# Optimization experiments

Measured on AMD Instinct MI355X. Metric: run time of the kernel, lower is better.

## Reference

```python
import jax, jax.numpy as jnp
import numpy as np

BATCH, SEQ, D_IN, D_OUT = 32, 1024, 128, 128
NEG_SLOPE = 0.1


def setup_inputs() -> dict:
    key = jax.random.key(0)
    k1, k2, k3, k4 = jax.random.split(key, 4)
    nodes = jax.random.normal(k1, (BATCH, SEQ, D_IN), dtype=jnp.float32)
    adjacent = jax.random.randint(k2, (BATCH, SEQ, SEQ), 0, 2, dtype=jnp.int32)
    W = jax.random.normal(k3, (D_IN, D_OUT), dtype=jnp.float32) / np.sqrt(D_IN)
    B = jax.random.normal(k4, (D_IN, D_OUT), dtype=jnp.float32) / np.sqrt(D_IN)
    return {"nodes": nodes, "adjacent": adjacent, "W": W, "B": B}


def reference(nodes, adjacent, W, B):
    # mask[b, out, in] = 1 if edge (out -> in) present
    mask = (adjacent != 0).astype(nodes.dtype)
    # counts[b, in] = in-degree (number of 'out' neighbors pooled per target node)
    counts = mask.sum(axis=1)                               # [b, s_in]
    # segment-sum of neighbor features: pooled[b, in, d] = sum_out mask * nodes[b, out, d]
    pooled = jnp.einsum('boi,bod->bid', mask, nodes)        # [b, s_in, d]
    # mean over neighbors; nodes with zero degree get no pooled contribution
    pooled = jnp.where(counts[..., None] > 0,
                       pooled / jnp.maximum(counts, 1.0)[..., None],
                       jnp.zeros((), dtype=nodes.dtype))
    updated = nodes @ B + pooled @ W                        # [b, s, d_out]
    return jax.nn.leaky_relu(updated, negative_slope=NEG_SLOPE)
```

## Files before the change

### kernel.cpp

```cpp
#include <hip/hip_runtime.h>
#include <hip/hip_bf16.h>

#define SEQ 1024
#define DIM 128
#define NEG_SLOPE 0.1f

typedef __bf16 bf16x8 __attribute__((ext_vector_type(8)));
typedef float f32x4v __attribute__((ext_vector_type(4)));
typedef unsigned char uchar;

#define NTQ_BYTES ((size_t)32 * 128 * 1024)

__device__ __forceinline__ unsigned short bfb(float f) {
    __bf16 h = (__bf16)f;
    return __builtin_bit_cast(unsigned short, h);
}

__device__ __forceinline__ uchar f32_to_e4m3(float f) {
#if __has_builtin(__builtin_amdgcn_cvt_pk_fp8_f32)
    int r = __builtin_amdgcn_cvt_pk_fp8_f32(f, f, 0, false);
    return (uchar)(r & 0xff);
#else
    unsigned u = __builtin_bit_cast(unsigned, f);
    unsigned s = (u >> 24) & 0x80;
    int e = (u >> 23) & 0xff;
    unsigned m = u & 0x7fffff;
    int te = e - 120;
    if (te >= 1) {
        unsigned keep = m >> 20, rest = m & 0xfffff;
        keep += (rest > 0x80000u) || (rest == 0x80000u && (keep & 1));
        if (keep == 8) { keep = 0; ++te; }
        if (te > 15) return (uchar)(s | 0x7e);
        return (uchar)(s | (te << 3) | keep);
    }
    float af = f < 0 ? -f : f;
    int q = (int)(af * 512.0f + 0.5f);
    if (q > 7) q = 7;
    return (uchar)(s | q);
#endif
}

__device__ __forceinline__ long mk64(unsigned lo, unsigned hi) {
    return (long)(((unsigned long long)hi << 32) | lo);
}

__global__ __launch_bounds__(256)
void transpose_nodes(const float* __restrict__ nodes, uchar* __restrict__ nq)
{
    __shared__ float lds[64][33];
    const int b  = blockIdx.x >> 6;
    const int ot = (blockIdx.x >> 2) & 15;
    const int dt = blockIdx.x & 3;
    const int o0 = ot << 6, d0 = dt << 5;
    const int t  = threadIdx.x;

    const float* src = nodes + ((size_t)(b * SEQ + o0)) * DIM + d0;
    #pragma unroll
    for (int p = 0; p < 8; ++p) {
        const int o = (t >> 5) + p * 8;
        const int d = t & 31;
        lds[o][d] = src[(size_t)o * DIM + d];
    }
    __syncthreads();

    const int d_loc = t >> 3;
    const int p0    = (t & 7) * 8;
    union { uchar b[8]; uint2 u; } pk;
    #pragma unroll
    for (int j = 0; j < 8; ++j) pk.b[j] = f32_to_e4m3(lds[p0 + j][d_loc]);
    *(uint2*)(nq + ((size_t)(b * DIM + d0 + d_loc)) * SEQ + o0 + p0) = pk.u;
}

__global__ __launch_bounds__(256)
void transpose_wb(const float* __restrict__ W, const float* __restrict__ Bm,
                  unsigned short* __restrict__ wt, unsigned short* __restrict__ bt)
{
    const int which = blockIdx.x & 1;
    const int slice = blockIdx.x >> 1;
    const float* in = which ? Bm : W;
    unsigned short* out = which ? bt : wt;
    const int base = slice * 1024;
    #pragma unroll
    for (int r = 0; r < 4; ++r) {
        const int idx = base + r * 256 + threadIdx.x;
        const int d = idx >> 7, k = idx & 127;
        out[idx] = bfb(in[k * DIM + d]);
    }
}

__global__ __launch_bounds__(256, 4)
void gcn_main(const float* __restrict__ nodes,
              const int* __restrict__ adj,
              const uchar* __restrict__ nq,
              const unsigned short* __restrict__ wt,
              const unsigned short* __restrict__ bt,
              float* __restrict__ out)
{
    __shared__ __align__(16) uchar mask_t[2][32][80];
    __shared__ unsigned short pooled[32][136];

    const int bid   = blockIdx.x;
    const int xcd   = bid & 7;
    const int slot  = bid >> 3;
    const int batch = ((slot >> 5) << 3) | xcd;
    const int itile = slot & 31;
    const int i0    = itile << 5;

    const int tid  = threadIdx.x;
    const int wave = tid >> 6;
    const int lane = tid & 63;
    const int wh   = wave >> 1;
    const int wn   = wave & 1;
    const int lrow = lane & 15;
    const int quad = lane >> 4;

    const int*   __restrict__ adj_b   = adj   + (size_t)batch * SEQ * SEQ;
    const uchar* __restrict__ nq_b    = nq    + (size_t)batch * DIM * SEQ;
    const float* __restrict__ nodes_b = nodes + (size_t)batch * SEQ * DIM;

    const int ig = tid & 15;
    const int og = tid >> 4;

    f32x4v acc[4] = {};
    f32x4v acc_cnt = {};
    const long ones = 0x3838383838383838L;

    int2 A[4];
    auto load_adj = [&](int oc) {
        const int* pa = adj_b + (size_t)(oc + og * 4) * SEQ + i0 + ig * 2;
        #pragma unroll
        for (int rr = 0; rr < 4; ++rr) A[rr] = *(const int2*)(pa + (size_t)rr * SEQ);
    };
    uint4 Bv[4];
    const uchar* pb0 = nq_b + (size_t)(wn * 64 + lrow) * SEQ + quad * 16;
    auto load_B = [&](int off) {
        #pragma unroll
        for (int nf = 0; nf < 4; ++nf)
            Bv[nf] = *(const uint4*)(pb0 + (size_t)nf * 16 * SEQ + off);
    };

    load_adj(0);
    load_B(0);

    for (int n = 0; n < 16; ++n) {
        const int buf = n & 1;
        unsigned w0 = 0, w1 = 0;
        #pragma unroll
        for (int rr = 0; rr < 4; ++rr) {
            w0 |= (A[rr].x != 0 ? 0x38u : 0u) << (8 * rr);
            w1 |= (A[rr].y != 0 ? 0x38u : 0u) << (8 * rr);
        }
        *(unsigned*)&mask_t[buf][ig * 2][og * 4]     = w0;
        *(unsigned*)&mask_t[buf][ig * 2 + 1][og * 4] = w1;
        __syncthreads();

        uint4 Bc[4];
        #pragma unroll
        for (int nf = 0; nf < 4; ++nf) Bc[nf] = Bv[nf];
        if (n < 15) {
            load_adj((n + 1) * 64);
            load_B((n + 1) * 64);
        }

        const uint4 a4 = *(const uint4*)&mask_t[buf][wh * 16 + lrow][quad * 16];
        #pragma unroll
        for (int half = 0; half < 2; ++half) {
            const long a64 = half ? mk64(a4.z, a4.w) : mk64(a4.x, a4.y);
            #pragma unroll
            for (int nf = 0; nf < 4; ++nf) {
                const long b64 = half ? mk64(Bc[nf].z, Bc[nf].w) : mk64(Bc[nf].x, Bc[nf].y);
                acc[nf] = __builtin_amdgcn_mfma_f32_16x16x32_fp8_fp8(a64, b64, acc[nf], 0, 0, 0);
            }
            acc_cnt = __builtin_amdgcn_mfma_f32_16x16x32_fp8_fp8(a64, ones, acc_cnt, 0, 0, 0);
        }
    }

    #pragma unroll
    for (int r = 0; r < 4; ++r) {
        const int row = wh * 16 + quad * 4 + r;
        const float cnt = acc_cnt[r];
        const float inv = (cnt > 0.5f) ? 1.0f / cnt : 0.0f;
        #pragma unroll
        for (int nf = 0; nf < 4; ++nf) {
            const int col = wn * 64 + nf * 16 + lrow;
            pooled[row][col] = bfb(acc[nf][r] * inv);
        }
    }
    __syncthreads();

    f32x4v acc2[4] = {};
    const int d_b0 = wn * 64 + lrow;

    #pragma unroll
    for (int ks = 0; ks < 4; ++ks) {
        const int k0 = ks * 32 + quad * 8;
        bf16x8 av, av2, bw[4], bb[4];
        av = *(const bf16x8*)&pooled[wh * 16 + lrow][k0];
        {
            const float* p = nodes_b + (size_t)(i0 + wh * 16 + lrow) * DIM + k0;
            const float4 f1 = *(const float4*)p;
            const float4 f2 = *(const float4*)(p + 4);
            av2[0] = (__bf16)f1.x; av2[1] = (__bf16)f1.y;
            av2[2] = (__bf16)f1.z; av2[3] = (__bf16)f1.w;
            av2[4] = (__bf16)f2.x; av2[5] = (__bf16)f2.y;
            av2[6] = (__bf16)f2.z; av2[7] = (__bf16)f2.w;
        }
        #pragma unroll
        for (int nf = 0; nf < 4; ++nf) {
            bw[nf] = *(const bf16x8*)(wt + (size_t)(d_b0 + nf * 16) * DIM + k0);
            bb[nf] = *(const bf16x8*)(bt + (size_t)(d_b0 + nf * 16) * DIM + k0);
        }
        #pragma unroll
        for (int nf = 0; nf < 4; ++nf) {
            acc2[nf] = __builtin_amdgcn_mfma_f32_16x16x32_bf16(av,  bw[nf], acc2[nf], 0, 0, 0);
            acc2[nf] = __builtin_amdgcn_mfma_f32_16x16x32_bf16(av2, bb[nf], acc2[nf], 0, 0, 0);
        }
    }

    float* out_b = out + (size_t)batch * SEQ * DIM;
    #pragma unroll
    for (int nf = 0; nf < 4; ++nf) {
        const int col = wn * 64 + nf * 16 + lrow;
        #pragma unroll
        for (int r = 0; r < 4; ++r) {
            const int row = i0 + wh * 16 + quad * 4 + r;
            const float x = acc2[nf][r];
            out_b[(size_t)row * DIM + col] = (x > 0.0f) ? x : NEG_SLOPE * x;
        }
    }
}

extern "C" void kernel_launch(void* const* d_in, const int* in_sizes, int n_in,
                              void* d_out, int out_size, void* d_ws, size_t ws_size,
                              hipStream_t stream) {
    const float* nodes = (const float*)d_in[0];
    const int*   adj   = (const int*)d_in[1];
    const float* W     = (const float*)d_in[2];
    const float* Bm    = (const float*)d_in[3];
    float*       out   = (float*)d_out;

    uchar* nq = (uchar*)d_ws;
    unsigned short* wt = (unsigned short*)(nq + NTQ_BYTES);
    unsigned short* bt = wt + 16384;

    transpose_nodes<<<dim3(2048), dim3(256), 0, stream>>>(nodes, nq);
    transpose_wb   <<<dim3(32),   dim3(256), 0, stream>>>(W, Bm, wt, bt);
    gcn_main       <<<dim3(1024), dim3(256), 0, stream>>>(nodes, adj, nq, wt, bt, out);
}
```

Baseline: 248.3 us.

## Stage full adjacency mask tile in LDS upfront, removing per-iteration barriers

The kernel now reads the block's whole 1024x32 adjacency column slab in a first phase, using 16-byte int4 loads instead of int2. It converts the slab to fp8 mask bytes and stores it transposed in a single LDS buffer that is unioned with the pooled tile. The MFMA loop then runs fully unrolled with no __syncthreads and only double-buffers the nq operand from global memory. The aim is to cut the 16 barriers and the fine-grained interleaving of adjacency loads. In exchange, LDS use rises to about 33KB per block, which may lower occupancy, and the adjacency load phase no longer overlaps with the MFMA work.

Result: no change. 252.9 us (+1.9%).

```diff
diff --git a/kernel.cpp b/kernel.cpp
--- a/kernel.cpp
+++ b/kernel.cpp
@@ -96,8 +96,11 @@
               const unsigned short* __restrict__ bt,
               float* __restrict__ out)
 {
-    __shared__ __align__(16) uchar mask_t[2][32][80];
-    __shared__ unsigned short pooled[32][136];
+    union U {
+        uchar maskT[32][1040];
+        unsigned short pooled[32][136];
+    };
+    __shared__ __align__(16) U u;
 
     const int bid   = blockIdx.x;
     const int xcd   = bid & 7;
@@ -118,51 +121,57 @@
     const uchar* __restrict__ nq_b    = nq    + (size_t)batch * DIM * SEQ;
     const float* __restrict__ nodes_b = nodes + (size_t)batch * SEQ * DIM;
 
-    const int ig = tid & 15;
-    const int og = tid >> 4;
+    const int cg = tid & 7;
+    const int rg = tid >> 3;
+    const int* pa_base = adj_b + (size_t)(rg * 4) * SEQ + i0 + cg * 4;
+
+    int4 Acur[4], Anxt[4];
+    #pragma unroll
+    for (int r = 0; r < 4; ++r) Acur[r] = *(const int4*)(pa_base + (size_t)r * SEQ);
+
+    #pragma unroll
+    for (int p = 0; p < 8; ++p) {
+        if (p < 7) {
+            const int* pa = pa_base + (size_t)(p + 1) * 128 * SEQ;
+            #pragma unroll
+            for (int r = 0; r < 4; ++r) Anxt[r] = *(const int4*)(pa + (size_t)r * SEQ);
+        }
+        const int obase = p * 128 + rg * 4;
+        #pragma unroll
+        for (int c = 0; c < 4; ++c) {
+            unsigned w = 0;
+            w |= (((const int*)&Acur[0])[c] != 0 ? 0x38u : 0u);
+            w |= (((const int*)&Acur[1])[c] != 0 ? 0x38u : 0u) << 8;
+            w |= (((const int*)&Acur[2])[c] != 0 ? 0x38u : 0u) << 16;
+            w |= (((const int*)&Acur[3])[c] != 0 ? 0x38u : 0u) << 24;
+            *(unsigned*)&u.maskT[cg * 4 + c][obase] = w;
+        }
+        #pragma unroll
+        for (int r = 0; r < 4; ++r) Acur[r] = Anxt[r];
+    }
+    __syncthreads();
 
     f32x4v acc[4] = {};
     f32x4v acc_cnt = {};
     const long ones = 0x3838383838383838L;
 
-    int2 A[4];
-    auto load_adj = [&](int oc) {
-        const int* pa = adj_b + (size_t)(oc + og * 4) * SEQ + i0 + ig * 2;
-        #pragma unroll
-        for (int rr = 0; rr < 4; ++rr) A[rr] = *(const int2*)(pa + (size_t)rr * SEQ);
-    };
-    uint4 Bv[4];
     const uchar* pb0 = nq_b + (size_t)(wn * 64 + lrow) * SEQ + quad * 16;
-    auto load_B = [&](int off) {
-        #pragma unroll
-        for (int nf = 0; nf < 4; ++nf)
-            Bv[nf] = *(const uint4*)(pb0 + (size_t)nf * 16 * SEQ + off);
-    };
-
-    load_adj(0);
-    load_B(0);
-
+    const uchar* prow = &u.maskT[wh * 16 + lrow][quad * 16];
+
+    uint4 Bbuf[2][4];
+    #pragma unroll
+    for (int nf = 0; nf < 4; ++nf)
+        Bbuf[0][nf] = *(const uint4*)(pb0 + (size_t)nf * 16 * SEQ);
+
+    #pragma unroll
     for (int n = 0; n < 16; ++n) {
-        const int buf = n & 1;
-        unsigned w0 = 0, w1 = 0;
-        #pragma unroll
-        for (int rr = 0; rr < 4; ++rr) {
-            w0 |= (A[rr].x != 0 ? 0x38u : 0u) << (8 * rr);
-            w1 |= (A[rr].y != 0 ? 0x38u : 0u) << (8 * rr);
-        }
-        *(unsigned*)&mask_t[buf][ig * 2][og * 4]     = w0;
-        *(unsigned*)&mask_t[buf][ig * 2 + 1][og * 4] = w1;
-        __syncthreads();
-
-        uint4 Bc[4];
-        #pragma unroll
-        for (int nf = 0; nf < 4; ++nf) Bc[nf] = Bv[nf];
         if (n < 15) {
-            load_adj((n + 1) * 64);
-            load_B((n + 1) * 64);
-        }
-
-        const uint4 a4 = *(const uint4*)&mask_t[buf][wh * 16 + lrow][quad * 16];
+            #pragma unroll
+            for (int nf = 0; nf < 4; ++nf)
+                Bbuf[(n + 1) & 1][nf] = *(const uint4*)(pb0 + (size_t)nf * 16 * SEQ + (n + 1) * 64);
+        }
+        const uint4 a4 = *(const uint4*)(prow + n * 64);
+        const uint4* Bc = Bbuf[n & 1];
         #pragma unroll
         for (int half = 0; half < 2; ++half) {
             const long a64 = half ? mk64(a4.z, a4.w) : mk64(a4.x, a4.y);
@@ -175,6 +184,8 @@
         }
     }
 
+    __syncthreads();
+
     #pragma unroll
     for (int r = 0; r < 4; ++r) {
         const int row = wh * 16 + quad * 4 + r;
@@ -183,7 +194,7 @@
         #pragma unroll
         for (int nf = 0; nf < 4; ++nf) {
             const int col = wn * 64 + nf * 16 + lrow;
-            pooled[row][col] = bfb(acc[nf][r] * inv);
+            u.pooled[row][col] = bfb(acc[nf][r] * inv);
         }
     }
     __syncthreads();
@@ -195,7 +206,7 @@
     for (int ks = 0; ks < 4; ++ks) {
         const int k0 = ks * 32 + quad * 8;
         bf16x8 av, av2, bw[4], bb[4];
-        av = *(const bf16x8*)&pooled[wh * 16 + lrow][k0];
+        av = *(const bf16x8*)&u.pooled[wh * 16 + lrow][k0];
         {
             const float* p = nodes_b + (size_t)(i0 + wh * 16 + lrow) * DIM + k0;
             const float4 f1 = *(const float4*)p;
```

## Pre-quantize adjacency to transposed fp8 mask in a separate kernel

Applied to the files above, without the earlier changes.

Adds a quant_adj kernel that reads the int32 adjacency once and writes a transposed fp8 mask (0x38 for an edge, 0 otherwise) to workspace. gcn_main then loads the A fragments straight from this byte mask. That drops the in-loop LDS transpose, the per-iteration __syncthreads, and the 4-byte adjacency reads in the main loop, and the loop now uses a three-slot register prefetch for both operands. In exchange there is an extra launch, about 64MB of extra traffic (32MB fp8 write plus 32MB read back), strided 16-byte writes in quant_adj, and the workspace must now hold the extra 32MB mask.

After: 311.2 us. 1.25x slower.

```diff
diff --git a/kernel.cpp b/kernel.cpp
--- a/kernel.cpp
+++ b/kernel.cpp
@@ -44,6 +44,33 @@
     return (long)(((unsigned long long)hi << 32) | lo);
 }
 
+__global__ __launch_bounds__(1024, 1)
+void quant_adj(const int* __restrict__ adj, uchar* __restrict__ mq)
+{
+    const int b  = blockIdx.x >> 3;
+    const int oc = blockIdx.x & 7;
+    const int t  = threadIdx.x;
+    const int* __restrict__ src = adj + ((size_t)b * SEQ + oc * 128) * SEQ + t;
+    uchar* dst = mq + ((size_t)b * SEQ + t) * SEQ + oc * 128;
+
+    #pragma unroll
+    for (int p = 0; p < 8; ++p) {
+        unsigned w[4];
+        #pragma unroll
+        for (int g = 0; g < 4; ++g) {
+            unsigned v = 0;
+            #pragma unroll
+            for (int j = 0; j < 4; ++j) {
+                const int x = src[(size_t)(p * 16 + g * 4 + j) * SEQ];
+                v |= (x != 0 ? 0x38u : 0u) << (8 * j);
+            }
+            w[g] = v;
+        }
+        uint4 o4; o4.x = w[0]; o4.y = w[1]; o4.z = w[2]; o4.w = w[3];
+        *(uint4*)(dst + p * 16) = o4;
+    }
+}
+
 __global__ __launch_bounds__(256)
 void transpose_nodes(const float* __restrict__ nodes, uchar* __restrict__ nq)
 {
@@ -90,13 +117,12 @@
 
 __global__ __launch_bounds__(256, 4)
 void gcn_main(const float* __restrict__ nodes,
-              const int* __restrict__ adj,
+              const uchar* __restrict__ mq,
               const uchar* __restrict__ nq,
               const unsigned short* __restrict__ wt,
               const unsigned short* __restrict__ bt,
               float* __restrict__ out)
 {
-    __shared__ __align__(16) uchar mask_t[2][32][80];
     __shared__ unsigned short pooled[32][136];
 
     const int bid   = blockIdx.x;
@@ -114,61 +140,43 @@
     const int lrow = lane & 15;
     const int quad = lane >> 4;
 
-    const int*   __restrict__ adj_b   = adj   + (size_t)batch * SEQ * SEQ;
-    const uchar* __restrict__ nq_b    = nq    + (size_t)batch * DIM * SEQ;
+    const uchar* __restrict__ mq_b    = mq + (size_t)batch * SEQ * SEQ;
+    const uchar* __restrict__ nq_b    = nq + (size_t)batch * DIM * SEQ;
     const float* __restrict__ nodes_b = nodes + (size_t)batch * SEQ * DIM;
-
-    const int ig = tid & 15;
-    const int og = tid >> 4;
 
     f32x4v acc[4] = {};
     f32x4v acc_cnt = {};
     const long ones = 0x3838383838383838L;
 
-    int2 A[4];
-    auto load_adj = [&](int oc) {
-        const int* pa = adj_b + (size_t)(oc + og * 4) * SEQ + i0 + ig * 2;
-        #pragma unroll
-        for (int rr = 0; rr < 4; ++rr) A[rr] = *(const int2*)(pa + (size_t)rr * SEQ);
-    };
-    uint4 Bv[4];
+    const uchar* pa0 = mq_b + (size_t)(i0 + wh * 16 + lrow) * SEQ + quad * 16;
     const uchar* pb0 = nq_b + (size_t)(wn * 64 + lrow) * SEQ + quad * 16;
-    auto load_B = [&](int off) {
+
+    uint4 Ab[3], Bb[3][4];
+    #pragma unroll
+    for (int k = 0; k < 2; ++k) {
+        Ab[k] = *(const uint4*)(pa0 + k * 64);
         #pragma unroll
         for (int nf = 0; nf < 4; ++nf)
-            Bv[nf] = *(const uint4*)(pb0 + (size_t)nf * 16 * SEQ + off);
-    };
-
-    load_adj(0);
-    load_B(0);
-
+            Bb[k][nf] = *(const uint4*)(pb0 + (size_t)nf * 16 * SEQ + k * 64);
+    }
+
+    #pragma unroll
     for (int n = 0; n < 16; ++n) {
-        const int buf = n & 1;
-        unsigned w0 = 0, w1 = 0;
-        #pragma unroll
-        for (int rr = 0; rr < 4; ++rr) {
-            w0 |= (A[rr].x != 0 ? 0x38u : 0u) << (8 * rr);
-            w1 |= (A[rr].y != 0 ? 0x38u : 0u) << (8 * rr);
-        }
-        *(unsigned*)&mask_t[buf][ig * 2][og * 4]     = w0;
-        *(unsigned*)&mask_t[buf][ig * 2 + 1][og * 4] = w1;
-        __syncthreads();
-
-        uint4 Bc[4];
-        #pragma unroll
-        for (int nf = 0; nf < 4; ++nf) Bc[nf] = Bv[nf];
-        if (n < 15) {
-            load_adj((n + 1) * 64);
-            load_B((n + 1) * 64);
-        }
-
-        const uint4 a4 = *(const uint4*)&mask_t[buf][wh * 16 + lrow][quad * 16];
+        if (n < 14) {
+            const int s = (n + 2) % 3;
+            Ab[s] = *(const uint4*)(pa0 + (n + 2) * 64);
+            #pragma unroll
+            for (int nf = 0; nf < 4; ++nf)
+                Bb[s][nf] = *(const uint4*)(pb0 + (size_t)nf * 16 * SEQ + (n + 2) * 64);
+        }
+        const uint4 a4 = Ab[n % 3];
         #pragma unroll
         for (int half = 0; half < 2; ++half) {
             const long a64 = half ? mk64(a4.z, a4.w) : mk64(a4.x, a4.y);
             #pragma unroll
             for (int nf = 0; nf < 4; ++nf) {
-                const long b64 = half ? mk64(Bc[nf].z, Bc[nf].w) : mk64(Bc[nf].x, Bc[nf].y);
+                const uint4 b4 = Bb[n % 3][nf];
+                const long b64 = half ? mk64(b4.z, b4.w) : mk64(b4.x, b4.y);
                 acc[nf] = __builtin_amdgcn_mfma_f32_16x16x32_fp8_fp8(a64, b64, acc[nf], 0, 0, 0);
             }
             acc_cnt = __builtin_amdgcn_mfma_f32_16x16x32_fp8_fp8(a64, ones, acc_cnt, 0, 0, 0);
@@ -242,8 +250,10 @@
     uchar* nq = (uchar*)d_ws;
     unsigned short* wt = (unsigned short*)(nq + NTQ_BYTES);
     unsigned short* bt = wt + 16384;
-
-    transpose_nodes<<<dim3(2048), dim3(256), 0, stream>>>(nodes, nq);
-    transpose_wb   <<<dim3(32),   dim3(256), 0, stream>>>(W, Bm, wt, bt);
-    gcn_main       <<<dim3(1024), dim3(256), 0, stream>>>(nodes, adj, nq, wt, bt, out);
-}
+    uchar* mq = (uchar*)(bt + 16384);
+
+    quant_adj      <<<dim3(256),  dim3(1024), 0, stream>>>(adj, mq);
+    transpose_nodes<<<dim3(2048), dim3(256),  0, stream>>>(nodes, nq);
+    transpose_wb   <<<dim3(32),   dim3(256),  0, stream>>>(W, Bm, wt, bt);
+    gcn_main       <<<dim3(1024), dim3(256),  0, stream>>>(nodes, mq, nq, wt, bt, out);
+}
```
